# Performance work log

Measured on AMD Instinct MI355X. Metric: run time of the kernel, lower is better.

Reference implementation:

```python
import jax, jax.numpy as jnp
import numpy as np

B, NCAMS = 1, 6
C_FEAT = 64                     # fusion_feat_in_dim
H, W = 88, 160                  # per-camera feature map size at fusion level
VOX_SIZE = (100, 100, 20)       # (x_dim, y_dim, z_dim) voxel counts
VOX_STR = (-50.0, -50.0, -15.0)
VOX_UNIT = (1.0, 1.0, 1.5)
N_VOX = VOX_SIZE[0] * VOX_SIZE[1] * VOX_SIZE[2]
EPS = 1e-8
V_PRE = 64                      # voxel_pre_dim[0]


def make_voxel_pts(dtype):
    # [B, 4, N]; homogeneous (x, y, z, 1) points, layout [z, y, x] flattened
    xs = jnp.linspace(VOX_STR[0], VOX_STR[0] + VOX_UNIT[0] * (VOX_SIZE[0] - 1), VOX_SIZE[0], dtype=dtype)
    ys = jnp.linspace(VOX_STR[1], VOX_STR[1] + VOX_UNIT[1] * (VOX_SIZE[1] - 1), VOX_SIZE[1], dtype=dtype)
    zs = jnp.linspace(VOX_STR[2], VOX_STR[2] + VOX_UNIT[2] * (VOX_SIZE[2] - 1), VOX_SIZE[2], dtype=dtype)
    zdim, ydim, xdim = VOX_SIZE[2], VOX_SIZE[1], VOX_SIZE[0]
    gx = jnp.broadcast_to(xs[None, None, :], (zdim, ydim, xdim)).reshape(-1)
    gy = jnp.broadcast_to(ys[None, :, None], (zdim, ydim, xdim)).reshape(-1)
    gz = jnp.broadcast_to(zs[:, None, None], (zdim, ydim, xdim)).reshape(-1)
    pts = jnp.stack([gx, gy, gz, jnp.ones_like(gx)], axis=0)  # [4, N]
    return jnp.broadcast_to(pts[None], (B, 4, N_VOX))


def _gather(imgf, iy, ix, Wd):
    # imgf: [BN, C, H*W]; iy/ix: [BN, N] int32 -> [BN, C, N]
    lin = iy * Wd + ix
    return jnp.take_along_axis(imgf, lin[:, None, :], axis=2)


def bilinear_sample(img, gx, gy):
    # grid_sample(mode='bilinear', padding_mode='zeros', align_corners=True)
    BN, C, Hd, Wd = img.shape
    x = (gx + 1.0) * 0.5 * (Wd - 1)
    y = (gy + 1.0) * 0.5 * (Hd - 1)
    x0 = jnp.floor(x); y0 = jnp.floor(y)
    wx1 = x - x0; wx0 = 1.0 - wx1
    wy1 = y - y0; wy0 = 1.0 - wy1
    imgf = img.reshape(BN, C, Hd * Wd)
    out = jnp.zeros((BN, C, gx.shape[1]), dtype=img.dtype)
    for xi, wxi in ((x0, wx0), (x0 + 1.0, wx1)):
        for yi, wyi in ((y0, wy0), (y0 + 1.0, wy1)):
            valid = (xi >= 0) & (xi <= Wd - 1) & (yi >= 0) & (yi <= Hd - 1)
            ii = jnp.clip(xi, 0, Wd - 1).astype(jnp.int32)
            jj = jnp.clip(yi, 0, Hd - 1).astype(jnp.int32)
            w = (wxi * wyi * valid.astype(img.dtype))[:, None, :]
            out = out + _gather(imgf, jj, ii, Wd) * w
    return out


def nearest_sample(img, gx, gy):
    # grid_sample(mode='nearest', padding_mode='zeros', align_corners=True)
    BN, C, Hd, Wd = img.shape
    x = (gx + 1.0) * 0.5 * (Wd - 1)
    y = (gy + 1.0) * 0.5 * (Hd - 1)
    xi = jnp.round(x); yi = jnp.round(y)
    valid = (xi >= 0) & (xi <= Wd - 1) & (yi >= 0) & (yi <= Hd - 1)
    ii = jnp.clip(xi, 0, Wd - 1).astype(jnp.int32)
    jj = jnp.clip(yi, 0, Hd - 1).astype(jnp.int32)
    imgf = img.reshape(BN, C, Hd * Wd)
    return _gather(imgf, jj, ii, Wd) * valid[:, None, :].astype(img.dtype)


def setup_inputs() -> dict:
    key = jax.random.key(0)
    ks = jax.random.split(key, 8)
    return {
        'multi_img_feat': jax.random.normal(ks[0], (B, NCAMS, C_FEAT, H, W), jnp.float32),
        'mask': jax.random.uniform(ks[1], (B, NCAMS, 1, H, W), jnp.float32),
        'K': jax.random.normal(ks[2], (B, NCAMS, 4, 4), jnp.float32),
        'extrinsics': jax.random.normal(ks[3], (B, NCAMS, 4, 4), jnp.float32),
        'w_no': jax.random.normal(ks[4], (V_PRE, C_FEAT + 1), jnp.float32) * 0.05,
        'b_no': jax.random.normal(ks[5], (V_PRE,), jnp.float32) * 0.05,
        'w_o': jax.random.normal(ks[6], (V_PRE, 2 * (C_FEAT + 1)), jnp.float32) * 0.05,
        'b_o': jax.random.normal(ks[7], (V_PRE,), jnp.float32) * 0.05,
    }


def reference(multi_img_feat, mask, K, extrinsics, w_no, b_no, w_o, b_o):
    Bb, NC, C, Hd, Wd = multi_img_feat.shape
    dt = multi_img_feat.dtype
    vpts = make_voxel_pts(dt)                                          # [B,4,N]
    vpts_c = jnp.broadcast_to(vpts[:, None], (Bb, NC, 4, N_VOX)).reshape(Bb * NC, 4, N_VOX)
    feats = multi_img_feat.reshape(Bb * NC, C, Hd, Wd)
    masks = mask.reshape(Bb * NC, 1, Hd, Wd)                           # interp to (H,W) is identity (same size, align_corners)
    ext = extrinsics.reshape(Bb * NC, 4, 4)[:, :3, :]
    K3 = K.reshape(Bb * NC, 4, 4)[:, :3, :3]

    v_local = jnp.einsum('bij,bjn->bin', ext, vpts_c)                  # [BN,3,N]
    cam_pts = jnp.einsum('bij,bjn->bin', K3, v_local)
    pix = cam_pts[:, :2] / (cam_pts[:, 2:3] + EPS)
    pix = jnp.where(jnp.all(jnp.isfinite(pix)), pix, jnp.clip(pix, -Wd * 2.0, Wd * 2.0))
    gx = (pix[:, 0] / (Wd - 1) - 0.5) * 2.0                            # [BN,N] normalized coords
    gy = (pix[:, 1] / (Hd - 1) - 0.5) * 2.0

    feat_w = bilinear_sample(feats, gx, gy)                            # [BN,C,N]
    m_occ = nearest_sample(masks, gx, gy) > 0.5                        # [BN,1,N]
    m_depth = v_local[:, 2:3] > 0
    oob = (gx > 1) | (gx < -1) | (gy > 1) | (gy < -1)
    valid = (m_occ & m_depth & (~oob)[:, None, :]).astype(dt)          # [BN,1,N]

    feat_w = jnp.concatenate([feat_w, v_local[:, 2:3] / VOX_SIZE[0]], axis=1) * valid  # [BN,C+1,N]

    feat_w = feat_w.reshape(Bb, NC, C + 1, N_VOX)
    valid = valid.reshape(Bb, NC, 1, N_VOX)
    count = valid.sum(axis=1)                                          # [B,1,N]

    # non-overlap branch: voxels seen by exactly one camera
    no_mask = (count == 1).astype(dt)
    vox_no = feat_w.sum(axis=1) * no_mask
    vox_no = jax.nn.elu(jnp.einsum('oc,bcn->bon', w_no, vox_no) + b_no[None, :, None]) * no_mask

    # overlap branch: cams {0,3,4} vs {1,2,5}
    o_mask = (count == 2).astype(dt)
    feat1 = feat_w[:, 0] + feat_w[:, 3] + feat_w[:, 4]
    feat2 = feat_w[:, 1] + feat_w[:, 2] + feat_w[:, 5]
    vox_o = jnp.concatenate([feat1, feat2], axis=1)                    # [B,2*(C+1),N]
    vox_o = jax.nn.elu(jnp.einsum('oc,bcn->bon', w_o, vox_o) + b_o[None, :, None]) * o_mask

    return vox_no + vox_o                                              # [B, V_PRE, N]
```

## Files before the change

kernel.cpp:

```cpp
#include <hip/hip_runtime.h>
#include <cmath>

#define NC 6
#define CF 64
#define HH 88
#define WW 160
#define NPIX 14080
#define NVOX 200000
#define VPRE 64
#define VB 128
#define NTH 512
#define NWV 8

typedef unsigned int u32;

__global__ __launch_bounds__(256) void transpose_feats(const float* __restrict__ in,
                                                       float* __restrict__ out) {
    __shared__ float tile[64 * 65];
    int blk = blockIdx.x;
    int c = blk / 220;
    int p0 = (blk - c * 220) * 64;
    int tid = threadIdx.x;
    int lane = tid & 63;
    int quad = tid >> 6;
    for (int r = quad; r < 64; r += 4)
        tile[r * 65 + lane] = in[(c * 64 + r) * NPIX + p0 + lane];
    __syncthreads();
    for (int r = quad; r < 64; r += 4)
        out[((c * NPIX) + p0 + r) * 64 + lane] = tile[lane * 65 + r];
}

__device__ __forceinline__ float elu1(float x) { return x > 0.0f ? x : expm1f(x); }

__device__ __forceinline__ float gather_bilin(const float* __restrict__ fsrc, int useT,
                                              int lane, int cam, float x, float y) {
    float x0f = floorf(x), y0f = floorf(y);
    float wx1 = x - x0f, wx0 = 1.0f - wx1;
    float wy1 = y - y0f, wy0 = 1.0f - wy1;
    float x1f = x0f + 1.0f, y1f = y0f + 1.0f;
    float bx0 = (x0f >= 0.0f && x0f <= 159.0f) ? 1.0f : 0.0f;
    float bx1 = (x1f >= 0.0f && x1f <= 159.0f) ? 1.0f : 0.0f;
    float by0 = (y0f >= 0.0f && y0f <= 87.0f) ? 1.0f : 0.0f;
    float by1 = (y1f >= 0.0f && y1f <= 87.0f) ? 1.0f : 0.0f;
    int ix0 = (int)fminf(fmaxf(x0f, 0.0f), 159.0f);
    int ix1 = (int)fminf(fmaxf(x1f, 0.0f), 159.0f);
    int iy0 = (int)fminf(fmaxf(y0f, 0.0f), 87.0f);
    int iy1 = (int)fminf(fmaxf(y1f, 0.0f), 87.0f);
    int A = useT ? 64 : 1;
    int Boff = useT ? (cam * NPIX * 64 + lane) : ((cam * 64 + lane) * NPIX);
    float v00 = fsrc[(iy0 * WW + ix0) * A + Boff];
    float v01 = fsrc[(iy1 * WW + ix0) * A + Boff];
    float v10 = fsrc[(iy0 * WW + ix1) * A + Boff];
    float v11 = fsrc[(iy1 * WW + ix1) * A + Boff];
    float fv;
    fv  = (wx0 * wy0 * bx0 * by0) * v00;
    fv += (wx0 * wy1 * bx0 * by1) * v01;
    fv += (wx1 * wy0 * bx1 * by0) * v10;
    fv += (wx1 * wy1 * bx1 * by1) * v11;
    return fv;
}

#define FMA8_STEP(W0,W1,W2,W3,W4,W5,W6,W7,CG,F0,F1,F2,F3) \
    a0 += W0[CG]*F0; a0 += W0[CG+1]*F1; a0 += W0[CG+2]*F2; a0 += W0[CG+3]*F3; \
    a1 += W1[CG]*F0; a1 += W1[CG+1]*F1; a1 += W1[CG+2]*F2; a1 += W1[CG+3]*F3; \
    a2 += W2[CG]*F0; a2 += W2[CG+1]*F1; a2 += W2[CG+2]*F2; a2 += W2[CG+3]*F3; \
    a3 += W3[CG]*F0; a3 += W3[CG+1]*F1; a3 += W3[CG+2]*F2; a3 += W3[CG+3]*F3; \
    a4 += W4[CG]*F0; a4 += W4[CG+1]*F1; a4 += W4[CG+2]*F2; a4 += W4[CG+3]*F3; \
    a5 += W5[CG]*F0; a5 += W5[CG+1]*F1; a5 += W5[CG+2]*F2; a5 += W5[CG+3]*F3; \
    a6 += W6[CG]*F0; a6 += W6[CG+1]*F1; a6 += W6[CG+2]*F2; a6 += W6[CG+3]*F3; \
    a7 += W7[CG]*F0; a7 += W7[CG+1]*F1; a7 += W7[CG+2]*F2; a7 += W7[CG+3]*F3;

__global__ __launch_bounds__(NTH, 4) void vox_main(
    const float* __restrict__ feats,
    const float* __restrict__ featT,
    const float* __restrict__ mask,
    const float* __restrict__ Kg,
    const float* __restrict__ ext,
    const float* __restrict__ wno,
    const float* __restrict__ bno,
    const float* __restrict__ wo,
    const float* __restrict__ bo,
    float* __restrict__ outp,
    int useT)
{
    __shared__ float s_ext[72];
    __shared__ float s_K[54];
    __shared__ __align__(16) float4 s_pair[NC * VB];
    __shared__ float s_F[65 * 66];
    __shared__ float s_stage[64 * 129];
    __shared__ u32 s_list1[VB], s_list2[VB];
    __shared__ int s_n1, s_n2;

    int tid = threadIdx.x;
    int lane = tid & 63;
    int wv = tid >> 6;
    int base = blockIdx.x * VB;

    if (tid == 0) { s_n1 = 0; s_n2 = 0; }
    if (tid >= 64 && tid < 136) {
        int i = tid - 64;
        s_ext[i] = ext[(i / 12) * 16 + (i % 12)];
    }
    if (tid >= 192 && tid < 246) {
        int i = tid - 192; int cam = i / 9; int e = i - cam * 9;
        s_K[i] = Kg[cam * 16 + (e / 3) * 4 + (e % 3)];
    }
    __syncthreads();

    for (int p = tid; p < NC * VB; p += NTH) {
        #pragma clang fp contract(off)
        int cam = p >> 7;
        int v = p & (VB - 1);
        int n = base + v;
        if (n < NVOX) {
            int xi = n % 100;
            int t = n / 100;
            int yi = t % 100;
            int zi = t / 100;
            float X = -50.0f + (float)xi;
            float Y = -50.0f + (float)yi;
            float Z = -15.0f + 1.5f * (float)zi;
            const float* E = s_ext + cam * 12;
            const float* Kk = s_K + cam * 9;
            float vl0 = E[0]*X + E[1]*Y + E[2]*Z + E[3];
            float vl1 = E[4]*X + E[5]*Y + E[6]*Z + E[7];
            float vl2 = E[8]*X + E[9]*Y + E[10]*Z + E[11];
            float c0 = Kk[0]*vl0 + Kk[1]*vl1 + Kk[2]*vl2;
            float c1 = Kk[3]*vl0 + Kk[4]*vl1 + Kk[5]*vl2;
            float c2 = Kk[6]*vl0 + Kk[7]*vl1 + Kk[8]*vl2;
            float pz = c2 + 1e-8f;
            float px = c0 / pz;
            float py = c1 / pz;
            float gx = (px / 159.0f - 0.5f) * 2.0f;
            float gy = (py / 87.0f - 0.5f) * 2.0f;
            float x = ((gx + 1.0f) * 0.5f) * 159.0f;
            float y = ((gy + 1.0f) * 0.5f) * 87.0f;
            float xr = rintf(x), yr = rintf(y);
            bool nv = (xr >= 0.0f) && (xr <= 159.0f) && (yr >= 0.0f) && (yr <= 87.0f);
            float mval = 0.0f;
            if (nv) mval = mask[(cam * HH + (int)yr) * WW + (int)xr];
            bool ok = (mval > 0.5f) && (vl2 > 0.0f) &&
                      !((gx > 1.0f) || (gx < -1.0f) || (gy > 1.0f) || (gy < -1.0f));
            s_pair[cam * VB + v] = make_float4(x, y, vl2, ok ? 1.0f : 0.0f);
        } else {
            s_pair[cam * VB + v] = make_float4(0.0f, 0.0f, 0.0f, 0.0f);
        }
    }
    __syncthreads();

    if (tid < VB) {
        int v = tid;
        const float* pw = (const float*)s_pair;
        int cnt = 0, cam0 = 0, cam1 = 0;
        #pragma unroll
        for (int c = 0; c < NC; ++c) {
            float w = pw[(c * VB + v) * 4 + 3];
            if (w != 0.0f) { if (cnt == 0) cam0 = c; else if (cnt == 1) cam1 = c; ++cnt; }
        }
        if (cnt == 1) {
            int s = atomicAdd(&s_n1, 1);
            s_list1[s] = (u32)(v | (cam0 << 8));
        } else if (cnt == 2) {
            int s = atomicAdd(&s_n2, 1);
            s_list2[s] = (u32)(v | (cam0 << 8) | (cam1 << 12));
        }
    }
    for (int i = tid; i < 64 * 129; i += NTH) s_stage[i] = 0.0f;
    __syncthreads();

    int n1 = s_n1, n2 = s_n2;
    const float* fsrc = useT ? featT : feats;
    int wvu = __builtin_amdgcn_readfirstlane(wv);
    int obase = wvu * 8;
    const float* w0n = wno + (obase + 0) * 65;
    const float* w1n = wno + (obase + 1) * 65;
    const float* w2n = wno + (obase + 2) * 65;
    const float* w3n = wno + (obase + 3) * 65;
    const float* w4n = wno + (obase + 4) * 65;
    const float* w5n = wno + (obase + 5) * 65;
    const float* w6n = wno + (obase + 6) * 65;
    const float* w7n = wno + (obase + 7) * 65;
    const float* w0o = wo + (obase + 0) * 130;
    const float* w1o = wo + (obase + 1) * 130;
    const float* w2o = wo + (obase + 2) * 130;
    const float* w3o = wo + (obase + 3) * 130;
    const float* w4o = wo + (obase + 4) * 130;
    const float* w5o = wo + (obase + 5) * 130;
    const float* w6o = wo + (obase + 6) * 130;
    const float* w7o = wo + (obase + 7) * 130;

    for (int t0 = 0; t0 < n1; t0 += 64) {
        int tl = min(64, n1 - t0);
        for (int e = wv; e < tl; e += NWV) {
            u32 ent = s_list1[t0 + e];
            int v = ent & 127, c = (ent >> 8) & 7;
            float4 pd = s_pair[c * VB + v];
            float fv = gather_bilin(fsrc, useT, lane, c, pd.x, pd.y);
            s_F[lane * 66 + e] = fv;
            if (lane == 0) s_F[64 * 66 + e] = pd.z / 100.0f;
        }
        __syncthreads();
        float a0 = bno[obase + 0], a1 = bno[obase + 1], a2 = bno[obase + 2], a3 = bno[obase + 3];
        float a4 = bno[obase + 4], a5 = bno[obase + 5], a6 = bno[obase + 6], a7 = bno[obase + 7];
        for (int cg = 0; cg < 64; cg += 4) {
            float f0 = s_F[(cg + 0) * 66 + lane];
            float f1 = s_F[(cg + 1) * 66 + lane];
            float f2 = s_F[(cg + 2) * 66 + lane];
            float f3 = s_F[(cg + 3) * 66 + lane];
            FMA8_STEP(w0n, w1n, w2n, w3n, w4n, w5n, w6n, w7n, cg, f0, f1, f2, f3)
        }
        float fd = s_F[64 * 66 + lane];
        a0 += w0n[64] * fd; a1 += w1n[64] * fd; a2 += w2n[64] * fd; a3 += w3n[64] * fd;
        a4 += w4n[64] * fd; a5 += w5n[64] * fd; a6 += w6n[64] * fd; a7 += w7n[64] * fd;
        if (lane < tl) {
            int vv = (int)(s_list1[t0 + lane] & 127);
            s_stage[(obase + 0) * 129 + vv] = elu1(a0);
            s_stage[(obase + 1) * 129 + vv] = elu1(a1);
            s_stage[(obase + 2) * 129 + vv] = elu1(a2);
            s_stage[(obase + 3) * 129 + vv] = elu1(a3);
            s_stage[(obase + 4) * 129 + vv] = elu1(a4);
            s_stage[(obase + 5) * 129 + vv] = elu1(a5);
            s_stage[(obase + 6) * 129 + vv] = elu1(a6);
            s_stage[(obase + 7) * 129 + vv] = elu1(a7);
        }
        __syncthreads();
    }

    for (int t0 = 0; t0 < n2; t0 += 64) {
        int tl = min(64, n2 - t0);
        for (int e = wv; e < tl; e += NWV) {
            u32 ent = s_list2[t0 + e];
            int v = ent & 127;
            int c0 = (ent >> 8) & 15, c1 = (ent >> 12) & 15;
            float fg = 0.0f, dd = 0.0f;
            if (!(c0 == 1 || c0 == 2 || c0 == 5)) {
                float4 pd = s_pair[c0 * VB + v];
                fg += gather_bilin(fsrc, useT, lane, c0, pd.x, pd.y);
                dd += pd.z / 100.0f;
            }
            if (!(c1 == 1 || c1 == 2 || c1 == 5)) {
                float4 pd = s_pair[c1 * VB + v];
                fg += gather_bilin(fsrc, useT, lane, c1, pd.x, pd.y);
                dd += pd.z / 100.0f;
            }
            s_F[lane * 66 + e] = fg;
            if (lane == 0) s_F[64 * 66 + e] = dd;
        }
        __syncthreads();
        float a0 = bo[obase + 0], a1 = bo[obase + 1], a2 = bo[obase + 2], a3 = bo[obase + 3];
        float a4 = bo[obase + 4], a5 = bo[obase + 5], a6 = bo[obase + 6], a7 = bo[obase + 7];
        for (int cg = 0; cg < 64; cg += 4) {
            float f0 = s_F[(cg + 0) * 66 + lane];
            float f1 = s_F[(cg + 1) * 66 + lane];
            float f2 = s_F[(cg + 2) * 66 + lane];
            float f3 = s_F[(cg + 3) * 66 + lane];
            FMA8_STEP(w0o, w1o, w2o, w3o, w4o, w5o, w6o, w7o, cg, f0, f1, f2, f3)
        }
        {
            float fd = s_F[64 * 66 + lane];
            a0 += w0o[64] * fd; a1 += w1o[64] * fd; a2 += w2o[64] * fd; a3 += w3o[64] * fd;
            a4 += w4o[64] * fd; a5 += w5o[64] * fd; a6 += w6o[64] * fd; a7 += w7o[64] * fd;
        }
        __syncthreads();
        for (int e = wv; e < tl; e += NWV) {
            u32 ent = s_list2[t0 + e];
            int v = ent & 127;
            int c0 = (ent >> 8) & 15, c1 = (ent >> 12) & 15;
            float fg = 0.0f, dd = 0.0f;
            if (c0 == 1 || c0 == 2 || c0 == 5) {
                float4 pd = s_pair[c0 * VB + v];
                fg += gather_bilin(fsrc, useT, lane, c0, pd.x, pd.y);
                dd += pd.z / 100.0f;
            }
            if (c1 == 1 || c1 == 2 || c1 == 5) {
                float4 pd = s_pair[c1 * VB + v];
                fg += gather_bilin(fsrc, useT, lane, c1, pd.x, pd.y);
                dd += pd.z / 100.0f;
            }
            s_F[lane * 66 + e] = fg;
            if (lane == 0) s_F[64 * 66 + e] = dd;
        }
        __syncthreads();
        for (int cg = 0; cg < 64; cg += 4) {
            float f0 = s_F[(cg + 0) * 66 + lane];
            float f1 = s_F[(cg + 1) * 66 + lane];
            float f2 = s_F[(cg + 2) * 66 + lane];
            float f3 = s_F[(cg + 3) * 66 + lane];
            int cgo = cg + 65;
            FMA8_STEP(w0o, w1o, w2o, w3o, w4o, w5o, w6o, w7o, cgo, f0, f1, f2, f3)
        }
        {
            float fd = s_F[64 * 66 + lane];
            a0 += w0o[129] * fd; a1 += w1o[129] * fd; a2 += w2o[129] * fd; a3 += w3o[129] * fd;
            a4 += w4o[129] * fd; a5 += w5o[129] * fd; a6 += w6o[129] * fd; a7 += w7o[129] * fd;
        }
        if (lane < tl) {
            int vv = (int)(s_list2[t0 + lane] & 127);
            s_stage[(obase + 0) * 129 + vv] = elu1(a0);
            s_stage[(obase + 1) * 129 + vv] = elu1(a1);
            s_stage[(obase + 2) * 129 + vv] = elu1(a2);
            s_stage[(obase + 3) * 129 + vv] = elu1(a3);
            s_stage[(obase + 4) * 129 + vv] = elu1(a4);
            s_stage[(obase + 5) * 129 + vv] = elu1(a5);
            s_stage[(obase + 6) * 129 + vv] = elu1(a6);
            s_stage[(obase + 7) * 129 + vv] = elu1(a7);
        }
        __syncthreads();
    }
    __syncthreads();

    for (int j = 0; j < 2; ++j) {
        int cb = base + j * 64;
        if (cb + lane < NVOX) {
            #pragma unroll
            for (int r8 = 0; r8 < 8; ++r8) {
                int r = wv * 8 + r8;
                outp[(size_t)r * NVOX + cb + lane] = s_stage[r * 129 + j * 64 + lane];
            }
        }
    }
}

extern "C" void kernel_launch(void* const* d_in, const int* in_sizes, int n_in,
                              void* d_out, int out_size, void* d_ws, size_t ws_size,
                              hipStream_t stream) {
    const float* feats = (const float*)d_in[0];
    const float* mask  = (const float*)d_in[1];
    const float* Kg    = (const float*)d_in[2];
    const float* ext   = (const float*)d_in[3];
    const float* wno   = (const float*)d_in[4];
    const float* bno   = (const float*)d_in[5];
    const float* wo    = (const float*)d_in[6];
    const float* bo    = (const float*)d_in[7];
    float* outp = (float*)d_out;
    float* featT = (float*)d_ws;

    size_t need = (size_t)NC * CF * NPIX * sizeof(float);
    int useT = (ws_size >= need) ? 1 : 0;
    if (useT) {
        transpose_feats<<<NC * 220, 256, 0, stream>>>(feats, featT);
    }
    int nblk = (NVOX + VB - 1) / VB;
    vox_main<<<nblk, NTH, 0, stream>>>(feats, featT, mask, Kg, ext,
                                       wno, bno, wo, bo, outp, useT);
}
```

Measured before the change: 170.9 us.

## Replace shared-memory output staging with pre-zeroed output and direct scattered stores

Drops the 33KB shared staging buffer, its zeroing and the final coalesced copy-out. A separate zero-fill kernel now clears the whole output first, and the main kernel writes only the active voxels straight to global memory with scattered stores. The freed LDS should allow higher occupancy, and inactive voxels no longer cost a store in the main kernel. In exchange, a full extra pass over the 51MB output is added, and the active-voxel writes become uncoalesced. The zero-fill relies on out_size being a multiple of four elements, which holds for 64x200000.

Result: faster. 165.8 us (-2.9%).

```diff
diff --git a/kernel.cpp b/kernel.cpp
--- a/kernel.cpp
+++ b/kernel.cpp
@@ -13,6 +13,12 @@
 #define NWV 8
 
 typedef unsigned int u32;
+
+__global__ __launch_bounds__(256) void zfill(float4* __restrict__ out, int n4) {
+    int i = blockIdx.x * 256 + threadIdx.x;
+    int stride = gridDim.x * 256;
+    for (; i < n4; i += stride) out[i] = make_float4(0.f, 0.f, 0.f, 0.f);
+}
 
 __global__ __launch_bounds__(256) void transpose_feats(const float* __restrict__ in,
                                                        float* __restrict__ out) {
@@ -87,7 +93,6 @@
     __shared__ float s_K[54];
     __shared__ __align__(16) float4 s_pair[NC * VB];
     __shared__ float s_F[65 * 66];
-    __shared__ float s_stage[64 * 129];
     __shared__ u32 s_list1[VB], s_list2[VB];
     __shared__ int s_n1, s_n2;
 
@@ -165,7 +170,6 @@
             s_list2[s] = (u32)(v | (cam0 << 8) | (cam1 << 12));
         }
     }
-    for (int i = tid; i < 64 * 129; i += NTH) s_stage[i] = 0.0f;
     __syncthreads();
 
     int n1 = s_n1, n2 = s_n2;
@@ -213,15 +217,15 @@
         a0 += w0n[64] * fd; a1 += w1n[64] * fd; a2 += w2n[64] * fd; a3 += w3n[64] * fd;
         a4 += w4n[64] * fd; a5 += w5n[64] * fd; a6 += w6n[64] * fd; a7 += w7n[64] * fd;
         if (lane < tl) {
-            int vv = (int)(s_list1[t0 + lane] & 127);
-            s_stage[(obase + 0) * 129 + vv] = elu1(a0);
-            s_stage[(obase + 1) * 129 + vv] = elu1(a1);
-            s_stage[(obase + 2) * 129 + vv] = elu1(a2);
-            s_stage[(obase + 3) * 129 + vv] = elu1(a3);
-            s_stage[(obase + 4) * 129 + vv] = elu1(a4);
-            s_stage[(obase + 5) * 129 + vv] = elu1(a5);
-            s_stage[(obase + 6) * 129 + vv] = elu1(a6);
-            s_stage[(obase + 7) * 129 + vv] = elu1(a7);
+            size_t col = (size_t)(base + (int)(s_list1[t0 + lane] & 127));
+            outp[(size_t)(obase + 0) * NVOX + col] = elu1(a0);
+            outp[(size_t)(obase + 1) * NVOX + col] = elu1(a1);
+            outp[(size_t)(obase + 2) * NVOX + col] = elu1(a2);
+            outp[(size_t)(obase + 3) * NVOX + col] = elu1(a3);
+            outp[(size_t)(obase + 4) * NVOX + col] = elu1(a4);
+            outp[(size_t)(obase + 5) * NVOX + col] = elu1(a5);
+            outp[(size_t)(obase + 6) * NVOX + col] = elu1(a6);
+            outp[(size_t)(obase + 7) * NVOX + col] = elu1(a7);
         }
         __syncthreads();
     }
@@ -295,29 +299,17 @@
             a4 += w4o[129] * fd; a5 += w5o[129] * fd; a6 += w6o[129] * fd; a7 += w7o[129] * fd;
         }
         if (lane < tl) {
-            int vv = (int)(s_list2[t0 + lane] & 127);
-            s_stage[(obase + 0) * 129 + vv] = elu1(a0);
-            s_stage[(obase + 1) * 129 + vv] = elu1(a1);
-            s_stage[(obase + 2) * 129 + vv] = elu1(a2);
-            s_stage[(obase + 3) * 129 + vv] = elu1(a3);
-            s_stage[(obase + 4) * 129 + vv] = elu1(a4);
-            s_stage[(obase + 5) * 129 + vv] = elu1(a5);
-            s_stage[(obase + 6) * 129 + vv] = elu1(a6);
-            s_stage[(obase + 7) * 129 + vv] = elu1(a7);
-        }
-        __syncthreads();
-    }
-    __syncthreads();
-
-    for (int j = 0; j < 2; ++j) {
-        int cb = base + j * 64;
-        if (cb + lane < NVOX) {
-            #pragma unroll
-            for (int r8 = 0; r8 < 8; ++r8) {
-                int r = wv * 8 + r8;
-                outp[(size_t)r * NVOX + cb + lane] = s_stage[r * 129 + j * 64 + lane];
-            }
-        }
+            size_t col = (size_t)(base + (int)(s_list2[t0 + lane] & 127));
+            outp[(size_t)(obase + 0) * NVOX + col] = elu1(a0);
+            outp[(size_t)(obase + 1) * NVOX + col] = elu1(a1);
+            outp[(size_t)(obase + 2) * NVOX + col] = elu1(a2);
+            outp[(size_t)(obase + 3) * NVOX + col] = elu1(a3);
+            outp[(size_t)(obase + 4) * NVOX + col] = elu1(a4);
+            outp[(size_t)(obase + 5) * NVOX + col] = elu1(a5);
+            outp[(size_t)(obase + 6) * NVOX + col] = elu1(a6);
+            outp[(size_t)(obase + 7) * NVOX + col] = elu1(a7);
+        }
+        __syncthreads();
     }
 }
 
@@ -335,6 +327,9 @@
     float* outp = (float*)d_out;
     float* featT = (float*)d_ws;
 
+    int n4 = out_size / 4;
+    zfill<<<2048, 256, 0, stream>>>((float4*)d_out, n4);
+
     size_t need = (size_t)NC * CF * NPIX * sizeof(float);
     int useT = (ws_size >= need) ? 1 : 0;
     if (useT) {
```
